# Kernel optimization log

Measured on AMD Instinct MI355X. Metric: run time of the kernel, lower is better.

Reference implementation:

```python
import jax, jax.numpy as jnp
import numpy as np

B, L = 1, 320
CS, CZ, CH, H, PQ, PV = 384, 128, 16, 12, 4, 8
INF, EPS = 1e5, 1e-8


def _quat_to_rot(q):
    w, x, y, z = q[..., 0], q[..., 1], q[..., 2], q[..., 3]
    r0 = jnp.stack([1 - 2*(y*y + z*z), 2*(x*y - w*z), 2*(x*z + w*y)], -1)
    r1 = jnp.stack([2*(x*y + w*z), 1 - 2*(x*x + z*z), 2*(y*z - w*x)], -1)
    r2 = jnp.stack([2*(x*z - w*y), 2*(y*z + w*x), 1 - 2*(x*x + y*y)], -1)
    return jnp.stack([r0, r1, r2], -2)


def setup_inputs():
    key = jax.random.key(0)
    ks = jax.random.split(key, 12)

    def lin(k, fan_in, fan_out):
        k1, k2 = jax.random.split(k)
        lim = 1.0 / np.sqrt(fan_in)
        return (jax.random.uniform(k1, (fan_in, fan_out), minval=-lim, maxval=lim, dtype=jnp.float32),
                jax.random.uniform(k2, (fan_out,), minval=-lim, maxval=lim, dtype=jnp.float32))

    s = jax.random.normal(ks[0], (B, L, CS), dtype=jnp.float32)
    quat = jax.random.normal(ks[1], (B, L, 4), dtype=jnp.float32)
    quat = quat / jnp.linalg.norm(quat, axis=-1, keepdims=True)
    rot = _quat_to_rot(quat)                                   # proper rotations (B,L,3,3)
    trans = 10.0 * jax.random.normal(ks[2], (B, L, 3), dtype=jnp.float32)
    z = jax.random.normal(ks[3], (B, L, L, CZ), dtype=jnp.float32)
    frame_mask = jnp.ones((B, L), dtype=jnp.float32)

    Wq, bq = lin(ks[4], CS, CH * H)
    Wkv, bkv = lin(ks[5], CS, 2 * CH * H)
    Wqp, bqp = lin(ks[6], CS, 6 * H * PQ)
    Wkvp, bkvp = lin(ks[7], CS, 6 * H * (PQ + PV))
    Wg, bg = lin(ks[8], CS, H * PQ)
    geom_weights = jnp.ones((3,), jnp.float32)
    dir_weight = jnp.asarray(0.5, jnp.float32)
    head_weights = 0.02 * jax.random.normal(ks[9], (H,), dtype=jnp.float32)
    concat_dim = H * (CH + 7 * PV) + H * CZ                    # 2400
    Wo, bo = lin(ks[10], concat_dim, CS)
    return dict(s=s, rot=rot, trans=trans, z=z, frame_mask=frame_mask,
                Wq=Wq, bq=bq, Wkv=Wkv, bkv=bkv, Wqp=Wqp, bqp=bqp,
                Wkvp=Wkvp, bkvp=bkvp, Wg=Wg, bg=bg,
                geom_weights=geom_weights, dir_weight=dir_weight,
                head_weights=head_weights, Wo=Wo, bo=bo)


def reference(s, rot, trans, z, frame_mask, Wq, bq, Wkv, bkv, Wqp, bqp,
              Wkvp, bkvp, Wg, bg, geom_weights, dir_weight, head_weights, Wo, bo):
    def proc_pts(pts_flat, P):
        # (B,L,6*H*P) -> rotate coords+translate, rotate dirs -> (B,L,H,P,6)
        pts = pts_flat.reshape(B, L, H, P, 6)
        coords = jnp.einsum('blij,blhpj->blhpi', rot, pts[..., :3]) + trans[:, :, None, None, :]
        dirs = jnp.einsum('blij,blhpj->blhpi', rot, pts[..., 3:])
        return jnp.concatenate([coords, dirs], -1)

    q = (s @ Wq + bq).reshape(B, L, H, CH)
    kv = s @ Wkv + bkv
    k = kv[..., :CH * H].reshape(B, L, H, CH)
    v = kv[..., CH * H:].reshape(B, L, H, CH)

    q_pts = proc_pts(s @ Wqp + bqp, PQ)
    kv_pts = s @ Wkvp + bkvp
    k_pts = proc_pts(kv_pts[..., :6 * H * PQ], PQ)
    v_pts = proc_pts(kv_pts[..., 6 * H * PQ:], PV)

    gate = jax.nn.sigmoid(s @ Wg + bg).reshape(B, L, H, PQ, 1)
    q_pts = q_pts * gate

    scalar_att = jnp.einsum('bqhc,bkhc->bhqk', q, k) / np.sqrt(CH).astype(np.float32)

    # position attention: per-pair point distances + log + inverse, mean over points
    delta = q_pts[:, :, None, :, :, :3] - k_pts[:, None, :, :, :, :3]   # (B,Lq,Lk,H,PQ,3)
    d = jnp.linalg.norm(delta, axis=-1)
    pos_att = (d + jnp.log(d + EPS) + 1.0 / (d + EPS)).mean(-1).transpose(0, 3, 1, 2)

    # direction attention: per-point dot minus cross-product 'curvature'
    qd, kd = q_pts[..., 3:], k_pts[..., 3:]
    dot = jnp.einsum('bqhpd,bkhpd->bqkhp', qd, kd)                       # (B,Lq,Lk,H,P)
    cr = jnp.cross(qd[:, :, None, :, None, :, :], kd[:, None, :, :, :, None, :])  # (B,Lq,Lk,H,Pk,Pq,3)
    cross = jnp.linalg.norm(cr, axis=-1).mean(-1)                        # (B,Lq,Lk,H,Pk)
    nq = jnp.linalg.norm(qd, axis=-1)[:, :, None]                        # (B,Lq,1,H,P)
    nk = jnp.linalg.norm(kd, axis=-1)[:, None]                           # (B,1,Lk,H,P)
    dir_att = (dot - cross / (nq * nk + EPS)).mean(-1).transpose(0, 3, 1, 2)

    att = scalar_att + dir_weight * (geom_weights[0] * pos_att + geom_weights[1] * dir_att)
    att = att * head_weights[:, None, None]
    mask2d = frame_mask[:, None, None, :] * frame_mask[:, None, :, None]  # (B,1,L,L)
    att = jax.nn.softmax(att + INF * (mask2d - 1.0), axis=-1)

    o_scalar = jnp.einsum('bhqk,bkhc->bqhc', att, v)
    o_geom = jnp.einsum('bhqk,bkhpd->bqhpd', att, v_pts)                 # (B,L,H,PV,6)

    # map aggregated geometry back into local frames
    rotT = jnp.swapaxes(rot, -1, -2)
    trans_inv = -jnp.einsum('blij,blj->bli', rotT, trans)
    lc = jnp.einsum('blij,blhpj->blhpi', rotT, o_geom[..., :3]) + trans_inv[:, :, None, None, :]
    ld = jnp.einsum('blij,blhpj->blhpi', rotT, o_geom[..., 3:6])
    ld = ld / jnp.maximum(jnp.linalg.norm(ld, axis=-1, keepdims=True), 1e-12)  # F.normalize
    ln = jnp.linalg.norm(lc, axis=-1, keepdims=True)
    o_geom7 = jnp.concatenate([lc, ld, ln], -1)                          # (B,L,H,PV,7)

    o_pair = jnp.einsum('bhij,bijk->bihk', att, z)                       # (B,L,H,CZ)
    out = jnp.concatenate([o_scalar.reshape(B, L, H * CH),
                           o_geom7.reshape(B, L, H * PV * 7),
                           o_pair.reshape(B, L, H * CZ)], -1)
    return out @ Wo + bo
```

## Files before the change

kernel.cpp:

```cpp
#include <hip/hip_runtime.h>
#include <hip/hip_bf16.h>
#include <math.h>

#define LSEQ 320
#define CS 384
#define CZ 128
#define CH 16
#define NH 12
#define PQ 4
#define PV 8
#define EPSF 1e-8f

typedef short short8 __attribute__((ext_vector_type(8)));
typedef float f32x4 __attribute__((ext_vector_type(4)));

__device__ __forceinline__ unsigned short f2b(float x) {
    union { float f; unsigned u; } v; v.f = x;
    unsigned r = (v.u + 0x7FFF + ((v.u >> 16) & 1)) >> 16;
    return (unsigned short)r;
}
__device__ __forceinline__ float b2f(unsigned short h) {
    union { unsigned u; float f; } v; v.u = ((unsigned)h) << 16;
    return v.f;
}

#define OFF_Q       0
#define OFF_KV      61440
#define OFF_QPT     184320
#define OFF_KPT     276480
#define OFF_KNRM    368640
#define OFF_ATTHI   552960
#define OFF_ATTLO   1372160
#define OFF_CCHI    2191360
#define OFF_CCLO    2575360
#define OFF_SHI     2959360
#define OFF_SMID    2990080
#define OFF_SLO     3020800
#define OFF_WCATHI  3051520
#define OFF_WCATMID 3392512
#define OFF_WCATLO  3733504
#define OFF_BCAT    4074496
#define OFF_WOHI    4076272
#define OFF_WOLO    4537072
#define OFF_VKVHI   4997872
#define OFF_VKVLO   5120752
#define OFF_QPR     5243632
#define OFF_KVPR    5335792
#define OFF_GATE    5612272
#define OFF_PART    5627632

__global__ __launch_bounds__(256) void k_cast(
    const float* __restrict__ s,
    const float* __restrict__ Wq, const float* __restrict__ bq,
    const float* __restrict__ Wkv, const float* __restrict__ bkv,
    const float* __restrict__ Wqp, const float* __restrict__ bqp,
    const float* __restrict__ Wkvp, const float* __restrict__ bkvp,
    const float* __restrict__ Wg, const float* __restrict__ bg,
    const float* __restrict__ Wo,
    unsigned short* __restrict__ s_hi, unsigned short* __restrict__ s_mid,
    unsigned short* __restrict__ s_lo,
    unsigned short* __restrict__ w_hi, unsigned short* __restrict__ w_mid,
    unsigned short* __restrict__ w_lo,
    float* __restrict__ bcat,
    unsigned short* __restrict__ wo_hi, unsigned short* __restrict__ wo_lo,
    float* __restrict__ ph_hi, float* __restrict__ ph_lo)
{
    int i = blockIdx.x * 256 + threadIdx.x;
    if (i < 122880) {
        float x = s[i];
        unsigned short hi = f2b(x);
        float r1 = x - b2f(hi);
        unsigned short mid = f2b(r1);
        s_hi[i] = hi; s_mid[i] = mid; s_lo[i] = f2b(r1 - b2f(mid));
        return;
    }
    i -= 122880;
    if (i < 681984) {
        int k = i / 1776, c = i - k * 1776;
        float v;
        if (c < 192)       v = Wq[(size_t)k * 192 + c];
        else if (c < 576)  v = Wkv[(size_t)k * 384 + c - 192];
        else if (c < 864)  v = Wqp[(size_t)k * 288 + c - 576];
        else if (c < 1728) v = Wkvp[(size_t)k * 864 + c - 864];
        else               v = Wg[(size_t)k * 48 + c - 1728];
        unsigned short hi = f2b(v);
        float r1 = v - b2f(hi);
        unsigned short mid = f2b(r1);
        w_hi[i] = hi; w_mid[i] = mid; w_lo[i] = f2b(r1 - b2f(mid));
        return;
    }
    i -= 681984;
    if (i < 1776) {
        float v;
        if (i < 192)       v = bq[i];
        else if (i < 576)  v = bkv[i - 192];
        else if (i < 864)  v = bqp[i - 576];
        else if (i < 1728) v = bkvp[i - 864];
        else               v = bg[i - 1728];
        bcat[i] = v;
        return;
    }
    i -= 1776;
    if (i < 921600) {
        float v = Wo[i];
        unsigned short hi = f2b(v);
        wo_hi[i] = hi; wo_lo[i] = f2b(v - b2f(hi));
        return;
    }
    i -= 921600;
    if (i < 204800) { ph_hi[i] = 0.0f; return; }
    i -= 204800;
    if (i < 204800) ph_lo[i] = 0.0f;
}

__global__ __launch_bounds__(256) void k_proj(
    const unsigned short* __restrict__ s_hi, const unsigned short* __restrict__ s_mid,
    const unsigned short* __restrict__ s_lo,
    const unsigned short* __restrict__ wc_hi, const unsigned short* __restrict__ wc_mid,
    const unsigned short* __restrict__ wc_lo,
    const float* __restrict__ bcat,
    float* __restrict__ qo, float* __restrict__ kvo,
    float* __restrict__ qpr, float* __restrict__ kvpr, float* __restrict__ gate)
{
    __shared__ unsigned short a_h[64][56], a_m[64][56], a_l[64][56];
    __shared__ unsigned short w_h[48][56], w_m[48][56], w_l[48][56];
    int col0 = blockIdx.x * 48, l0 = blockIdx.y * 64;
    int tid = threadIdx.x;
    int lane = tid & 63, w = tid >> 6;
    int ncol = lane & 15, blk = lane >> 4, mrow = (lane >> 4) * 4;

    float* dst; int nc, cbase; bool sig = false;
    if (col0 < 192)       { nc = 192; cbase = col0;        dst = qo;   }
    else if (col0 < 576)  { nc = 384; cbase = col0 - 192;  dst = kvo;  }
    else if (col0 < 864)  { nc = 288; cbase = col0 - 576;  dst = qpr;  }
    else if (col0 < 1728) { nc = 864; cbase = col0 - 864;  dst = kvpr; }
    else                  { nc = 48;  cbase = 0;           dst = gate; sig = true; }

    f32x4 acc[3] = {};
    for (int k0 = 0; k0 < 384; k0 += 32) {
        __syncthreads();
        {
            int row = tid >> 2, seg = tid & 3;
            size_t off = (size_t)(l0 + row) * 384 + k0 + seg * 8;
            *(short8*)&a_h[row][seg * 8] = *(const short8*)(s_hi + off);
            *(short8*)&a_m[row][seg * 8] = *(const short8*)(s_mid + off);
            *(short8*)&a_l[row][seg * 8] = *(const short8*)(s_lo + off);
        }
        if (tid < 96) {
            int kk = tid / 3, coff = (tid % 3) * 16;
            size_t off = (size_t)(k0 + kk) * 1776 + col0 + coff;
            short8 h0 = *(const short8*)(wc_hi + off);
            short8 h1 = *(const short8*)(wc_hi + off + 8);
            short8 m0 = *(const short8*)(wc_mid + off);
            short8 m1 = *(const short8*)(wc_mid + off + 8);
            short8 l0v = *(const short8*)(wc_lo + off);
            short8 l1v = *(const short8*)(wc_lo + off + 8);
            #pragma unroll
            for (int i = 0; i < 8; i++) {
                w_h[coff + i][kk]     = (unsigned short)h0[i];
                w_h[coff + 8 + i][kk] = (unsigned short)h1[i];
                w_m[coff + i][kk]     = (unsigned short)m0[i];
                w_m[coff + 8 + i][kk] = (unsigned short)m1[i];
                w_l[coff + i][kk]     = (unsigned short)l0v[i];
                w_l[coff + 8 + i][kk] = (unsigned short)l1v[i];
            }
        }
        __syncthreads();
        short8 afh = *(short8*)&a_h[w * 16 + ncol][blk * 8];
        short8 afm = *(short8*)&a_m[w * 16 + ncol][blk * 8];
        short8 afl = *(short8*)&a_l[w * 16 + ncol][blk * 8];
        #pragma unroll
        for (int s3 = 0; s3 < 3; s3++) {
            short8 bfh = *(short8*)&w_h[s3 * 16 + ncol][blk * 8];
            short8 bfm = *(short8*)&w_m[s3 * 16 + ncol][blk * 8];
            short8 bfl = *(short8*)&w_l[s3 * 16 + ncol][blk * 8];
            acc[s3] = __builtin_amdgcn_mfma_f32_16x16x32_bf16(afm, bfm, acc[s3], 0, 0, 0);
            acc[s3] = __builtin_amdgcn_mfma_f32_16x16x32_bf16(afh, bfl, acc[s3], 0, 0, 0);
            acc[s3] = __builtin_amdgcn_mfma_f32_16x16x32_bf16(afl, bfh, acc[s3], 0, 0, 0);
            acc[s3] = __builtin_amdgcn_mfma_f32_16x16x32_bf16(afh, bfm, acc[s3], 0, 0, 0);
            acc[s3] = __builtin_amdgcn_mfma_f32_16x16x32_bf16(afm, bfh, acc[s3], 0, 0, 0);
            acc[s3] = __builtin_amdgcn_mfma_f32_16x16x32_bf16(afh, bfh, acc[s3], 0, 0, 0);
        }
    }
    #pragma unroll
    for (int s3 = 0; s3 < 3; s3++) {
        float bv = bcat[col0 + s3 * 16 + ncol];
        int cloc = cbase + s3 * 16 + ncol;
        #pragma unroll
        for (int r = 0; r < 4; r++) {
            float v2 = acc[s3][r] + bv;
            if (sig) v2 = 1.0f / (1.0f + expf(-v2));
            dst[(size_t)(l0 + w * 16 + mrow + r) * nc + cloc] = v2;
        }
    }
}

__global__ __launch_bounds__(256) void k_points(
    const float* __restrict__ qpr, const float* __restrict__ kvpr, const float* __restrict__ gate,
    const float* __restrict__ rot, const float* __restrict__ trans,
    const float* __restrict__ kv,
    float* __restrict__ qpt, float* __restrict__ kpt, float* __restrict__ knrm,
    unsigned short* __restrict__ vkv_hi, unsigned short* __restrict__ vkv_lo)
{
    __shared__ float vsh[96][6];
    int l = blockIdx.x, t = threadIdx.x;
    const float* R = rot + l * 9;
    float tx = trans[l * 3], ty = trans[l * 3 + 1], tz = trans[l * 3 + 2];
    if (t < 192) {
        const float* src; float g = 1.0f; float* dst = nullptr; int vj = -1;
        if (t < 48)      { src = qpr + (size_t)l * 288 + t * 6; g = gate[l * 48 + t]; dst = qpt + ((size_t)l * 48 + t) * 6; }
        else if (t < 96) { int j = t - 48; src = kvpr + (size_t)l * 864 + j * 6; dst = kpt + ((size_t)l * 48 + j) * 6; }
        else             { int j = t - 96; src = kvpr + (size_t)l * 864 + 288 + j * 6; vj = j; }
        float px = src[0], py = src[1], pz = src[2], ux = src[3], uy = src[4], uz = src[5];
        float c0 = R[0] * px + R[1] * py + R[2] * pz + tx;
        float c1 = R[3] * px + R[4] * py + R[5] * pz + ty;
        float c2 = R[6] * px + R[7] * py + R[8] * pz + tz;
        float d0 = R[0] * ux + R[1] * uy + R[2] * uz;
        float d1 = R[3] * ux + R[4] * uy + R[5] * uz;
        float d2 = R[6] * ux + R[7] * uy + R[8] * uz;
        if (vj >= 0) {
            vsh[vj][0] = c0; vsh[vj][1] = c1; vsh[vj][2] = c2;
            vsh[vj][3] = d0; vsh[vj][4] = d1; vsh[vj][5] = d2;
        } else {
            dst[0] = c0 * g; dst[1] = c1 * g; dst[2] = c2 * g;
            dst[3] = d0 * g; dst[4] = d1 * g; dst[5] = d2 * g;
            if (t >= 48) {
                knrm[(size_t)(t - 48) * 320 + l] = sqrtf(d0 * d0 + d1 * d1 + d2 * d2);
            }
        }
    }
    __syncthreads();
    #pragma unroll
    for (int e = 0; e < 3; e++) {
        int u = t * 3 + e;
        int h = u >> 6, n = u & 63;
        float val;
        if (n < 16) val = kv[(size_t)l * 384 + 192 + h * 16 + n];
        else        val = vsh[h * 8 + (n - 16) / 6][(n - 16) % 6];
        unsigned short hi = f2b(val);
        size_t idx = ((size_t)h * 64 + n) * 320 + l;
        vkv_hi[idx] = hi;
        vkv_lo[idx] = f2b(val - b2f(hi));
    }
}

__global__ __launch_bounds__(256) void k_att(
    const float* __restrict__ qb, const float* __restrict__ kvb,
    const float* __restrict__ qpt, const float* __restrict__ kpt,
    const float* __restrict__ knrm,
    const float* __restrict__ fm, const float* __restrict__ gw,
    const float* __restrict__ dwp, const float* __restrict__ hwp,
    unsigned short* __restrict__ att_hi, unsigned short* __restrict__ att_lo)
{
    __shared__ float kp_sh[320][45];
    int tid = threadIdx.x;
    int w = tid >> 6, lane = tid & 63;
    int iq = blockIdx.x * 4 + w;
    int h = blockIdx.y;

    for (int idx = tid; idx < 320 * 44; idx += 256) {
        int kk = idx / 44, j = idx - kk * 44;
        float v;
        if (j < 24)      v = kpt[(size_t)kk * 288 + h * 24 + j];
        else if (j < 40) v = kvb[(size_t)kk * 384 + h * 16 + (j - 24)];
        else             v = knrm[(size_t)(h * 4 + (j - 40)) * 320 + kk];
        kp_sh[kk][j] = v;
    }
    __syncthreads();

    float qv[CH];
    #pragma unroll
    for (int c = 0; c < CH; c++) qv[c] = qb[(size_t)iq * 192 + h * CH + c];
    float qp[24];
    #pragma unroll
    for (int j = 0; j < 24; j++) qp[j] = qpt[(size_t)iq * 288 + h * 24 + j];
    float nq[PQ], nq2[PQ];
    #pragma unroll
    for (int p = 0; p < PQ; p++) {
        float x = qp[p * 6 + 3], y = qp[p * 6 + 4], zz = qp[p * 6 + 5];
        nq2[p] = x * x + y * y + zz * zz;
        nq[p] = sqrtf(nq2[p]);
    }
    float dwv = dwp[0], g0 = gw[0], g1 = gw[1], hwv = hwp[h];
    float fmi = fm[iq];

    float lg[5];
    #pragma unroll
    for (int r = 0; r < 5; r++) {
        int kk = r * 64 + lane;
        const float* row = &kp_sh[kk][0];

        float scalar = 0.f;
        #pragma unroll
        for (int c = 0; c < CH; c++) scalar += qv[c] * row[24 + c];
        scalar *= 0.25f;

        float pos = 0.f;
        #pragma unroll
        for (int p = 0; p < PQ; p++) {
            float dx = qp[p * 6] - row[p * 6];
            float dy = qp[p * 6 + 1] - row[p * 6 + 1];
            float dz = qp[p * 6 + 2] - row[p * 6 + 2];
            float d = __builtin_amdgcn_sqrtf(dx * dx + dy * dy + dz * dz);
            float de = d + EPSF;
            pos += d + __logf(de) + __builtin_amdgcn_rcpf(de);
        }
        pos *= 0.25f;

        float dir = 0.f;
        #pragma unroll
        for (int p = 0; p < PQ; p++) {
            float kx = row[p * 6 + 3], ky = row[p * 6 + 4], kz = row[p * 6 + 5];
            float nk = row[40 + p];
            float nk2 = nk * nk;
            float cm = 0.f, dself = 0.f;
            #pragma unroll
            for (int pq = 0; pq < PQ; pq++) {
                float dq = qp[pq * 6 + 3] * kx + qp[pq * 6 + 4] * ky + qp[pq * 6 + 5] * kz;
                if (pq == p) dself = dq;
                cm += __builtin_amdgcn_sqrtf(fmaxf(nq2[pq] * nk2 - dq * dq, 0.0f));
            }
            cm *= 0.25f;
            dir += dself - cm * __builtin_amdgcn_rcpf(nq[p] * nk + EPSF);
        }
        dir *= 0.25f;

        float logit = scalar + dwv * (g0 * pos + g1 * dir);
        logit *= hwv;
        logit += 100000.0f * (fmi * fm[kk] - 1.0f);
        lg[r] = logit;
    }

    float mx = lg[0];
    #pragma unroll
    for (int r = 1; r < 5; r++) mx = fmaxf(mx, lg[r]);
    for (int m = 32; m; m >>= 1) mx = fmaxf(mx, __shfl_xor(mx, m, 64));

    float e[5], sm = 0.f;
    #pragma unroll
    for (int r = 0; r < 5; r++) { e[r] = __expf(lg[r] - mx); sm += e[r]; }
    for (int m = 32; m; m >>= 1) sm += __shfl_xor(sm, m, 64);
    float inv = 1.0f / sm;
    #pragma unroll
    for (int r = 0; r < 5; r++) {
        float p = e[r] * inv;
        unsigned short hi = f2b(p);
        size_t idx = ((size_t)h * 320 + iq) * 320 + r * 64 + lane;
        att_hi[idx] = hi;
        att_lo[idx] = f2b(p - b2f(hi));
    }
}

__global__ __launch_bounds__(64) void k_sv(
    const unsigned short* __restrict__ att_hi, const unsigned short* __restrict__ att_lo,
    const unsigned short* __restrict__ vkv_hi, const unsigned short* __restrict__ vkv_lo,
    const float* __restrict__ rot, const float* __restrict__ trans,
    unsigned short* __restrict__ cc_hi, unsigned short* __restrict__ cc_lo)
{
    __shared__ unsigned short a_hi[16][56];
    __shared__ unsigned short a_lo[16][56];
    __shared__ unsigned short bt_hi[64][56];
    __shared__ unsigned short bt_lo[64][56];
    __shared__ float ogsh[16][49];
    int iq0 = blockIdx.x * 16, h = blockIdx.y;
    int tid = threadIdx.x;
    int ncol = tid & 15, blk = tid >> 4, mrow = (tid >> 4) * 4;

    f32x4 acc[4] = {};
    for (int k0 = 0; k0 < 320; k0 += 32) {
        __syncthreads();
        {
            int row = tid >> 2, seg = tid & 3;
            size_t off = ((size_t)h * 320 + iq0 + row) * 320 + k0 + seg * 8;
            *(short8*)&a_hi[row][seg * 8] = *(const short8*)(att_hi + off);
            *(short8*)&a_lo[row][seg * 8] = *(const short8*)(att_lo + off);
        }
        {
            size_t off = ((size_t)h * 64 + tid) * 320 + k0;
            #pragma unroll
            for (int j2 = 0; j2 < 4; j2++) {
                *(short8*)&bt_hi[tid][j2 * 8] = *(const short8*)(vkv_hi + off + j2 * 8);
                *(short8*)&bt_lo[tid][j2 * 8] = *(const short8*)(vkv_lo + off + j2 * 8);
            }
        }
        __syncthreads();
        short8 afh = *(short8*)&a_hi[ncol][blk * 8];
        short8 afl = *(short8*)&a_lo[ncol][blk * 8];
        #pragma unroll
        for (int s4 = 0; s4 < 4; s4++) {
            short8 bfh = *(short8*)&bt_hi[s4 * 16 + ncol][blk * 8];
            short8 bfl = *(short8*)&bt_lo[s4 * 16 + ncol][blk * 8];
            acc[s4] = __builtin_amdgcn_mfma_f32_16x16x32_bf16(afh, bfh, acc[s4], 0, 0, 0);
            acc[s4] = __builtin_amdgcn_mfma_f32_16x16x32_bf16(afh, bfl, acc[s4], 0, 0, 0);
            acc[s4] = __builtin_amdgcn_mfma_f32_16x16x32_bf16(afl, bfh, acc[s4], 0, 0, 0);
        }
    }
    #pragma unroll
    for (int s4 = 0; s4 < 4; s4++) {
        int n = s4 * 16 + ncol;
        #pragma unroll
        for (int r = 0; r < 4; r++) {
            int iq = iq0 + mrow + r;
            float v = acc[s4][r];
            if (n < 16) {
                unsigned short hi = f2b(v);
                size_t idx = (size_t)iq * 2400 + h * 16 + n;
                cc_hi[idx] = hi;
                cc_lo[idx] = f2b(v - b2f(hi));
            } else {
                ogsh[mrow + r][n - 16] = v;
            }
        }
    }
    __syncthreads();
    #pragma unroll
    for (int t2 = tid; t2 < 128; t2 += 64) {
        int iqr = t2 >> 3, p = t2 & 7;
        int l = iq0 + iqr;
        const float* R = rot + l * 9;
        float tx = trans[l * 3], ty = trans[l * 3 + 1], tz = trans[l * 3 + 2];
        const float* o = &ogsh[iqr][p * 6];
        float gx = o[0] - tx, gy = o[1] - ty, gz = o[2] - tz;
        float l0 = R[0] * gx + R[3] * gy + R[6] * gz;
        float l1 = R[1] * gx + R[4] * gy + R[7] * gz;
        float l2 = R[2] * gx + R[5] * gy + R[8] * gz;
        float dx = o[3], dy = o[4], dz = o[5];
        float e0 = R[0] * dx + R[3] * dy + R[6] * dz;
        float e1 = R[1] * dx + R[4] * dy + R[7] * dz;
        float e2 = R[2] * dx + R[5] * dy + R[8] * dz;
        float n = sqrtf(e0 * e0 + e1 * e1 + e2 * e2);
        float inv = 1.0f / fmaxf(n, 1e-12f);
        float ln = sqrtf(l0 * l0 + l1 * l1 + l2 * l2);
        float vals[7] = { l0, l1, l2, e0 * inv, e1 * inv, e2 * inv, ln };
        size_t base = (size_t)l * 2400 + 192 + (h * PV + p) * 7;
        #pragma unroll
        for (int j = 0; j < 7; j++) {
            unsigned short hi = f2b(vals[j]);
            cc_hi[base + j] = hi;
            cc_lo[base + j] = f2b(vals[j] - b2f(hi));
        }
    }
}

__global__ __launch_bounds__(256) void k_pair(
    const unsigned short* __restrict__ att_hi, const unsigned short* __restrict__ att_lo,
    const float* __restrict__ z,
    unsigned short* __restrict__ cc_hi, unsigned short* __restrict__ cc_lo)
{
    __shared__ unsigned short a_hi[16][56];
    __shared__ unsigned short a_lo[16][56];
    __shared__ unsigned short zt_sh[128][56];
    int iq = blockIdx.x;
    int tid = threadIdx.x;
    int lane = tid & 63, w = tid >> 6;
    int ncol = lane & 15, blk = lane >> 4, mrow = (lane >> 4) * 4;

    f32x4 acc[2] = {};
    for (int k0 = 0; k0 < 320; k0 += 32) {
        __syncthreads();
        if (tid < 64) {
            int row = tid >> 2, seg = tid & 3;
            size_t off = (size_t)row * 102400 + (size_t)iq * 320 + k0 + seg * 8;
            *(short8*)&a_hi[row][seg * 8] = *(const short8*)(att_hi + off);
            *(short8*)&a_lo[row][seg * 8] = *(const short8*)(att_lo + off);
        }
        {
            int kk = tid >> 3, cb = (tid & 7) * 16;
            const float* src = z + ((size_t)iq * 320 + k0 + kk) * 128 + cb;
            #pragma unroll
            for (int g4 = 0; g4 < 4; g4++) {
                float4 f = *(const float4*)(src + g4 * 4);
                zt_sh[cb + g4 * 4 + 0][kk] = f2b(f.x);
                zt_sh[cb + g4 * 4 + 1][kk] = f2b(f.y);
                zt_sh[cb + g4 * 4 + 2][kk] = f2b(f.z);
                zt_sh[cb + g4 * 4 + 3][kk] = f2b(f.w);
            }
        }
        __syncthreads();
        short8 afh = *(short8*)&a_hi[ncol][blk * 8];
        short8 afl = *(short8*)&a_lo[ncol][blk * 8];
        #pragma unroll
        for (int s2 = 0; s2 < 2; s2++) {
            short8 bf = *(short8*)&zt_sh[w * 32 + s2 * 16 + ncol][blk * 8];
            acc[s2] = __builtin_amdgcn_mfma_f32_16x16x32_bf16(afl, bf, acc[s2], 0, 0, 0);
            acc[s2] = __builtin_amdgcn_mfma_f32_16x16x32_bf16(afh, bf, acc[s2], 0, 0, 0);
        }
    }
    #pragma unroll
    for (int s2 = 0; s2 < 2; s2++) {
        int n = w * 32 + s2 * 16 + ncol;
        #pragma unroll
        for (int r = 0; r < 4; r++) {
            int h = mrow + r;
            if (h < 12) {
                float v = acc[s2][r];
                unsigned short hi = f2b(v);
                size_t idx = (size_t)iq * 2400 + 864 + h * 128 + n;
                cc_hi[idx] = hi;
                cc_lo[idx] = f2b(v - b2f(hi));
            }
        }
    }
}

__global__ __launch_bounds__(256) void k_gemm(
    const unsigned short* __restrict__ cc_hi, const unsigned short* __restrict__ cc_lo,
    const unsigned short* __restrict__ wo_hi, const unsigned short* __restrict__ wo_lo,
    float* __restrict__ part)
{
    __shared__ unsigned short a_hi[64][56];
    __shared__ unsigned short a_lo[64][56];
    __shared__ unsigned short w_hi[48][56];
    __shared__ unsigned short w_lo[48][56];
    int iq0 = blockIdx.x * 64, col0 = blockIdx.y * 48, ks = blockIdx.z;
    int tid = threadIdx.x;
    int lane = tid & 63, w = tid >> 6;
    int ncol = lane & 15, blk = lane >> 4, mrow = (lane >> 4) * 4;

    f32x4 acc[3] = {};
    for (int kc = 0; kc < 15; kc++) {
        int k0 = ks * 480 + kc * 32;
        __syncthreads();
        {
            int row = tid >> 2, seg = tid & 3;
            size_t off = (size_t)(iq0 + row) * 2400 + k0 + seg * 8;
            *(short8*)&a_hi[row][seg * 8] = *(const short8*)(cc_hi + off);
            *(short8*)&a_lo[row][seg * 8] = *(const short8*)(cc_lo + off);
        }
        if (tid < 96) {
            int kk = tid / 3, coff = (tid % 3) * 16;
            size_t off = (size_t)(k0 + kk) * 384 + col0 + coff;
            short8 h0 = *(const short8*)(wo_hi + off);
            short8 h1 = *(const short8*)(wo_hi + off + 8);
            short8 l0v = *(const short8*)(wo_lo + off);
            short8 l1v = *(const short8*)(wo_lo + off + 8);
            #pragma unroll
            for (int i = 0; i < 8; i++) {
                w_hi[coff + i][kk]     = (unsigned short)h0[i];
                w_hi[coff + 8 + i][kk] = (unsigned short)h1[i];
                w_lo[coff + i][kk]     = (unsigned short)l0v[i];
                w_lo[coff + 8 + i][kk] = (unsigned short)l1v[i];
            }
        }
        __syncthreads();
        short8 afh = *(short8*)&a_hi[w * 16 + ncol][blk * 8];
        short8 afl = *(short8*)&a_lo[w * 16 + ncol][blk * 8];
        #pragma unroll
        for (int s3 = 0; s3 < 3; s3++) {
            short8 bfh = *(short8*)&w_hi[s3 * 16 + ncol][blk * 8];
            short8 bfl = *(short8*)&w_lo[s3 * 16 + ncol][blk * 8];
            acc[s3] = __builtin_amdgcn_mfma_f32_16x16x32_bf16(afh, bfh, acc[s3], 0, 0, 0);
            acc[s3] = __builtin_amdgcn_mfma_f32_16x16x32_bf16(afh, bfl, acc[s3], 0, 0, 0);
            acc[s3] = __builtin_amdgcn_mfma_f32_16x16x32_bf16(afl, bfh, acc[s3], 0, 0, 0);
        }
    }
    #pragma unroll
    for (int s3 = 0; s3 < 3; s3++) {
        int cn = col0 + s3 * 16 + ncol;
        #pragma unroll
        for (int r = 0; r < 4; r++)
            part[((size_t)ks * 320 + iq0 + w * 16 + mrow + r) * 384 + cn] = acc[s3][r];
    }
}

__global__ __launch_bounds__(256) void k_reduce(
    const float* __restrict__ part, const float* __restrict__ bo, float* __restrict__ out)
{
    int i = blockIdx.x * 256 + threadIdx.x;
    float v = bo[i % CS];
    #pragma unroll
    for (int ks = 0; ks < 5; ks++) v += part[(size_t)ks * 122880 + i];
    out[i] = v;
}

extern "C" void kernel_launch(void* const* d_in, const int* in_sizes, int n_in,
                              void* d_out, int out_size, void* d_ws, size_t ws_size,
                              hipStream_t stream)
{
    const float* s     = (const float*)d_in[0];
    const float* rot   = (const float*)d_in[1];
    const float* trans = (const float*)d_in[2];
    const float* z     = (const float*)d_in[3];
    const float* fm    = (const float*)d_in[4];
    const float* Wq    = (const float*)d_in[5];
    const float* bq    = (const float*)d_in[6];
    const float* Wkv   = (const float*)d_in[7];
    const float* bkv   = (const float*)d_in[8];
    const float* Wqp   = (const float*)d_in[9];
    const float* bqp   = (const float*)d_in[10];
    const float* Wkvp  = (const float*)d_in[11];
    const float* bkvp  = (const float*)d_in[12];
    const float* Wg    = (const float*)d_in[13];
    const float* bg    = (const float*)d_in[14];
    const float* gw    = (const float*)d_in[15];
    const float* dw    = (const float*)d_in[16];
    const float* hw    = (const float*)d_in[17];
    const float* Wo    = (const float*)d_in[18];
    const float* bo    = (const float*)d_in[19];

    float* ws = (float*)d_ws;
    float*          q       = ws + OFF_Q;
    float*          kv      = ws + OFF_KV;
    float*          qpt     = ws + OFF_QPT;
    float*          kpt     = ws + OFF_KPT;
    float*          knrm    = ws + OFF_KNRM;
    unsigned short* att_hi  = (unsigned short*)(ws + OFF_ATTHI);
    unsigned short* att_lo  = (unsigned short*)(ws + OFF_ATTLO);
    float*          ph_hi   = ws + OFF_ATTHI + 12 * 51200;
    float*          ph_lo   = ws + OFF_ATTLO + 12 * 51200;
    unsigned short* cc_hi   = (unsigned short*)(ws + OFF_CCHI);
    unsigned short* cc_lo   = (unsigned short*)(ws + OFF_CCLO);
    unsigned short* s_hi    = (unsigned short*)(ws + OFF_SHI);
    unsigned short* s_mid   = (unsigned short*)(ws + OFF_SMID);
    unsigned short* s_lo    = (unsigned short*)(ws + OFF_SLO);
    unsigned short* wc_hi   = (unsigned short*)(ws + OFF_WCATHI);
    unsigned short* wc_mid  = (unsigned short*)(ws + OFF_WCATMID);
    unsigned short* wc_lo   = (unsigned short*)(ws + OFF_WCATLO);
    float*          bcat    = ws + OFF_BCAT;
    unsigned short* wo_hi   = (unsigned short*)(ws + OFF_WOHI);
    unsigned short* wo_lo   = (unsigned short*)(ws + OFF_WOLO);
    unsigned short* vkv_hi  = (unsigned short*)(ws + OFF_VKVHI);
    unsigned short* vkv_lo  = (unsigned short*)(ws + OFF_VKVLO);
    float*          qpr     = ws + OFF_QPR;
    float*          kvpr    = ws + OFF_KVPR;
    float*          gate    = ws + OFF_GATE;
    float*          part    = ws + OFF_PART;
    float* out = (float*)d_out;

    k_cast<<<dim3(8352), dim3(256), 0, stream>>>(s, Wq, bq, Wkv, bkv, Wqp, bqp,
                                                 Wkvp, bkvp, Wg, bg, Wo,
                                                 s_hi, s_mid, s_lo, wc_hi, wc_mid, wc_lo,
                                                 bcat, wo_hi, wo_lo, ph_hi, ph_lo);
    k_proj<<<dim3(37, 5), dim3(256), 0, stream>>>(s_hi, s_mid, s_lo, wc_hi, wc_mid, wc_lo,
                                                  bcat, q, kv, qpr, kvpr, gate);
    k_points<<<dim3(LSEQ), dim3(256), 0, stream>>>(qpr, kvpr, gate, rot, trans, kv,
                                                   qpt, kpt, knrm, vkv_hi, vkv_lo);
    k_att<<<dim3(80, NH), dim3(256), 0, stream>>>(q, kv, qpt, kpt, knrm, fm, gw, dw, hw,
                                                  att_hi, att_lo);
    k_sv<<<dim3(20, NH), dim3(64), 0, stream>>>(att_hi, att_lo, vkv_hi, vkv_lo,
                                                rot, trans, cc_hi, cc_lo);
    k_pair<<<dim3(LSEQ), dim3(256), 0, stream>>>(att_hi, att_lo, z, cc_hi, cc_lo);
    k_gemm<<<dim3(5, 8, 5), dim3(256), 0, stream>>>(cc_hi, cc_lo, wo_hi, wo_lo, part);
    k_reduce<<<dim3(480), dim3(256), 0, stream>>>(part, bo, out);
}
```

Before: 234.1 us.

## Pack per-head key rows in k_points and read them directly in k_att

k_points now writes a packed per-head key record (points, scalar keys, direction norms, padded to 48 floats) laid out as [head][key][48]. k_att drops its shared-memory staging of all 320 keys per block and the barrier, and reads each key row straight from global memory through the cache. This removes the repeated gather and transpose across 80 blocks per head and cuts LDS usage, at the cost of per-lane strided global reads during the logit loop. It also relies on the workspace being large enough for the new OFF_KROW region.

After: 219.2 us. 1.07x faster.

```diff
diff --git a/kernel.cpp b/kernel.cpp
--- a/kernel.cpp
+++ b/kernel.cpp
@@ -27,8 +27,6 @@
 #define OFF_Q       0
 #define OFF_KV      61440
 #define OFF_QPT     184320
-#define OFF_KPT     276480
-#define OFF_KNRM    368640
 #define OFF_ATTHI   552960
 #define OFF_ATTLO   1372160
 #define OFF_CCHI    2191360
@@ -48,6 +46,7 @@
 #define OFF_KVPR    5335792
 #define OFF_GATE    5612272
 #define OFF_PART    5627632
+#define OFF_KROW    6242032
 
 __global__ __launch_bounds__(256) void k_cast(
     const float* __restrict__ s,
@@ -199,17 +198,19 @@
     const float* __restrict__ qpr, const float* __restrict__ kvpr, const float* __restrict__ gate,
     const float* __restrict__ rot, const float* __restrict__ trans,
     const float* __restrict__ kv,
-    float* __restrict__ qpt, float* __restrict__ kpt, float* __restrict__ knrm,
+    float* __restrict__ qpt, float* __restrict__ krow,
     unsigned short* __restrict__ vkv_hi, unsigned short* __restrict__ vkv_lo)
 {
     __shared__ float vsh[96][6];
+    __shared__ float kp_s[48][6];
+    __shared__ float kn_s[48];
     int l = blockIdx.x, t = threadIdx.x;
     const float* R = rot + l * 9;
     float tx = trans[l * 3], ty = trans[l * 3 + 1], tz = trans[l * 3 + 2];
     if (t < 192) {
-        const float* src; float g = 1.0f; float* dst = nullptr; int vj = -1;
+        const float* src; float g = 1.0f; float* dst = nullptr; int vj = -1, kj = -1;
         if (t < 48)      { src = qpr + (size_t)l * 288 + t * 6; g = gate[l * 48 + t]; dst = qpt + ((size_t)l * 48 + t) * 6; }
-        else if (t < 96) { int j = t - 48; src = kvpr + (size_t)l * 864 + j * 6; dst = kpt + ((size_t)l * 48 + j) * 6; }
+        else if (t < 96) { kj = t - 48; src = kvpr + (size_t)l * 864 + kj * 6; }
         else             { int j = t - 96; src = kvpr + (size_t)l * 864 + 288 + j * 6; vj = j; }
         float px = src[0], py = src[1], pz = src[2], ux = src[3], uy = src[4], uz = src[5];
         float c0 = R[0] * px + R[1] * py + R[2] * pz + tx;
@@ -221,12 +222,13 @@
         if (vj >= 0) {
             vsh[vj][0] = c0; vsh[vj][1] = c1; vsh[vj][2] = c2;
             vsh[vj][3] = d0; vsh[vj][4] = d1; vsh[vj][5] = d2;
+        } else if (kj >= 0) {
+            kp_s[kj][0] = c0; kp_s[kj][1] = c1; kp_s[kj][2] = c2;
+            kp_s[kj][3] = d0; kp_s[kj][4] = d1; kp_s[kj][5] = d2;
+            kn_s[kj] = sqrtf(d0 * d0 + d1 * d1 + d2 * d2);
         } else {
             dst[0] = c0 * g; dst[1] = c1 * g; dst[2] = c2 * g;
             dst[3] = d0 * g; dst[4] = d1 * g; dst[5] = d2 * g;
-            if (t >= 48) {
-                knrm[(size_t)(t - 48) * 320 + l] = sqrtf(d0 * d0 + d1 * d1 + d2 * d2);
-            }
         }
     }
     __syncthreads();
@@ -242,32 +244,29 @@
         vkv_hi[idx] = hi;
         vkv_lo[idx] = f2b(val - b2f(hi));
     }
+    for (int idx = t; idx < 576; idx += 256) {
+        int h = idx / 48, j = idx - h * 48;
+        float v;
+        if (j < 24)      v = kp_s[h * 4 + j / 6][j % 6];
+        else if (j < 40) v = kv[(size_t)l * 384 + h * 16 + (j - 24)];
+        else if (j < 44) v = kn_s[h * 4 + (j - 40)];
+        else             v = 0.0f;
+        krow[((size_t)h * 320 + l) * 48 + j] = v;
+    }
 }
 
 __global__ __launch_bounds__(256) void k_att(
-    const float* __restrict__ qb, const float* __restrict__ kvb,
-    const float* __restrict__ qpt, const float* __restrict__ kpt,
-    const float* __restrict__ knrm,
+    const float* __restrict__ qb, const float* __restrict__ qpt,
+    const float* __restrict__ krow,
     const float* __restrict__ fm, const float* __restrict__ gw,
     const float* __restrict__ dwp, const float* __restrict__ hwp,
     unsigned short* __restrict__ att_hi, unsigned short* __restrict__ att_lo)
 {
-    __shared__ float kp_sh[320][45];
     int tid = threadIdx.x;
     int w = tid >> 6, lane = tid & 63;
     int iq = blockIdx.x * 4 + w;
     int h = blockIdx.y;
 
-    for (int idx = tid; idx < 320 * 44; idx += 256) {
-        int kk = idx / 44, j = idx - kk * 44;
-        float v;
-        if (j < 24)      v = kpt[(size_t)kk * 288 + h * 24 + j];
-        else if (j < 40) v = kvb[(size_t)kk * 384 + h * 16 + (j - 24)];
-        else             v = knrm[(size_t)(h * 4 + (j - 40)) * 320 + kk];
-        kp_sh[kk][j] = v;
-    }
-    __syncthreads();
-
     float qv[CH];
     #pragma unroll
     for (int c = 0; c < CH; c++) qv[c] = qb[(size_t)iq * 192 + h * CH + c];
@@ -288,7 +287,7 @@
     #pragma unroll
     for (int r = 0; r < 5; r++) {
         int kk = r * 64 + lane;
-        const float* row = &kp_sh[kk][0];
+        const float* row = krow + ((size_t)h * 320 + kk) * 48;
 
         float scalar = 0.f;
         #pragma unroll
@@ -602,8 +601,6 @@
     float*          q       = ws + OFF_Q;
     float*          kv      = ws + OFF_KV;
     float*          qpt     = ws + OFF_QPT;
-    float*          kpt     = ws + OFF_KPT;
-    float*          knrm    = ws + OFF_KNRM;
     unsigned short* att_hi  = (unsigned short*)(ws + OFF_ATTHI);
     unsigned short* att_lo  = (unsigned short*)(ws + OFF_ATTLO);
     float*          ph_hi   = ws + OFF_ATTHI + 12 * 51200;
@@ -625,6 +622,7 @@
     float*          kvpr    = ws + OFF_KVPR;
     float*          gate    = ws + OFF_GATE;
     float*          part    = ws + OFF_PART;
+    float*          krow    = ws + OFF_KROW;
     float* out = (float*)d_out;
 
     k_cast<<<dim3(8352), dim3(256), 0, stream>>>(s, Wq, bq, Wkv, bkv, Wqp, bqp,
@@ -634,8 +632,8 @@
     k_proj<<<dim3(37, 5), dim3(256), 0, stream>>>(s_hi, s_mid, s_lo, wc_hi, wc_mid, wc_lo,
                                                   bcat, q, kv, qpr, kvpr, gate);
     k_points<<<dim3(LSEQ), dim3(256), 0, stream>>>(qpr, kvpr, gate, rot, trans, kv,
-                                                   qpt, kpt, knrm, vkv_hi, vkv_lo);
-    k_att<<<dim3(80, NH), dim3(256), 0, stream>>>(q, kv, qpt, kpt, knrm, fm, gw, dw, hw,
+                                                   qpt, krow, vkv_hi, vkv_lo);
+    k_att<<<dim3(80, NH), dim3(256), 0, stream>>>(q, qpt, krow, fm, gw, dw, hw,
                                                   att_hi, att_lo);
     k_sv<<<dim3(20, NH), dim3(64), 0, stream>>>(att_hi, att_lo, vkv_hi, vkv_lo,
                                                 rot, trans, cc_hi, cc_lo);
```
